# Kernel optimization log

Hardware: AMD Instinct MI355X
Metric: run time of the kernel (lower is better)

## Reference

```python
import jax, jax.numpy as jnp
import numpy as np

B, NQ, NK = 16, 1024, 1024
DQ = DK = DV = 512
H = 4
DH = DV // H  # 128


def layer_norm(x, g, b, eps=1e-5):
    mu = jnp.mean(x, axis=-1, keepdims=True)
    var = jnp.var(x, axis=-1, keepdims=True)  # biased, matches torch LayerNorm
    return (x - mu) / jnp.sqrt(var + eps) * g + b


def setup_inputs() -> dict:
    key = jax.random.key(0)
    ks = jax.random.split(key, 16)
    s = lambda d: 1.0 / np.sqrt(d)
    return {
        "Q": jax.random.normal(ks[0], (B, NQ, DQ), jnp.float32),
        "K": jax.random.normal(ks[1], (B, NK, DK), jnp.float32),
        "weights": jax.random.uniform(ks[2], (H * B, NQ, NK), jnp.float32),
        "Wq": jax.random.normal(ks[3], (DV, DQ), jnp.float32) * s(DQ),
        "bq": jnp.zeros((DV,), jnp.float32),
        "Wk": jax.random.normal(ks[4], (DV, DK), jnp.float32) * s(DK),
        "bk": jnp.zeros((DV,), jnp.float32),
        "Wv": jax.random.normal(ks[5], (DV, DK), jnp.float32) * s(DK),
        "bv": jnp.zeros((DV,), jnp.float32),
        "Wo": jax.random.normal(ks[6], (DV, DV), jnp.float32) * s(DV),
        "bo": jnp.zeros((DV,), jnp.float32),
        "g0": jnp.ones((DV,), jnp.float32),
        "beta0": jnp.zeros((DV,), jnp.float32),
        "g1": jnp.ones((DV,), jnp.float32),
        "beta1": jnp.zeros((DV,), jnp.float32),
    }


def reference(Q, K, weights, Wq, bq, Wk, bk, Wv, bv, Wo, bo, g0, beta0, g1, beta1):
    q = Q @ Wq.T + bq  # [B,NQ,DV]
    k = K @ Wk.T + bk  # [B,NK,DV]
    v = K @ Wv.T + bv  # [B,NK,DV]

    # torch split(dh, 2) + cat(0) == head-major [H,B,N,DH]
    def heads(x, n):
        return x.reshape(B, n, H, DH).transpose(2, 0, 1, 3)

    q_, k_, v_ = heads(q, NQ), heads(k, NK), heads(v, NK)

    # NOTE: original scales by sqrt(dim_V), not sqrt(head_dim)
    scores = jnp.einsum("hbqd,hbkd->hbqk", q_, k_) / np.sqrt(DV)
    log_w = jnp.log(jnp.clip(weights, 0.0, None)).reshape(H, B, NQ, NK)
    A = jax.nn.softmax(scores + log_w, axis=-1)  # [H,B,NQ,NK]

    o = q_ + jnp.einsum("hbqk,hbkd->hbqd", A, v_)  # residual inside heads
    # split(B,0)+cat(2) == merge heads back to [B,NQ,DV]
    O = o.transpose(1, 2, 0, 3).reshape(B, NQ, DV)
    O = layer_norm(O, g0, beta0)
    O = O + jax.nn.relu(O @ Wo.T + bo)
    O = layer_norm(O, g1, beta1)
    return O
```

## Files before the change

kernel.cpp:

```cpp
#include <hip/hip_runtime.h>

typedef unsigned short u16;
typedef unsigned int u32;
typedef __attribute__((ext_vector_type(8))) short short8;
typedef __attribute__((ext_vector_type(4))) float f32x4;
typedef __attribute__((ext_vector_type(2))) u32 uintx2;
typedef __attribute__((address_space(3))) u32 lds32;
typedef const __attribute__((address_space(1))) u32 g32c;

__device__ __forceinline__ u16 f2bf(float f) {
  union { float f; u32 u; } v; v.f = f;
  return (u16)((v.u + 0x7fffu + ((v.u >> 16) & 1u)) >> 16);
}
__device__ __forceinline__ float bf2f(u16 h) {
  union { u32 u; float f; } v; v.u = ((u32)h) << 16;
  return v.f;
}

__global__ void cvt_w_kernel(const float* __restrict__ Wq, const float* __restrict__ Wk,
                             const float* __restrict__ Wv, const float* __restrict__ Wo,
                             u16* __restrict__ dst) {
  int m = blockIdx.y;
  const float* s = (m == 0) ? Wq : (m == 1) ? Wk : (m == 2) ? Wv : Wo;
  int idx = (blockIdx.x * 256 + threadIdx.x) * 4;
  float4 v = *(const float4*)(s + idx);
  uintx2 pk;
  pk[0] = (u32)f2bf(v.x) | ((u32)f2bf(v.y) << 16);
  pk[1] = (u32)f2bf(v.z) | ((u32)f2bf(v.w) << 16);
  *(uintx2*)(dst + m * 262144 + idx) = pk;
}

template <bool AF32, bool OUTMODE, bool TRANSV>
__device__ __forceinline__ void gemm_bt_body(const void* __restrict__ Ap,
                                             const u16* __restrict__ Bw,
                                             const float* __restrict__ bias,
                                             u16* __restrict__ C) {
  __shared__ u16 ldsA[128 * 64];
  __shared__ u16 ldsB[128 * 64];
  const int t = threadIdx.x;
  const int lane = t & 63, wid = t >> 6;
  const int lr = lane & 15, lg = lane >> 4;
  const int n0 = blockIdx.x * 128;
  const int m0 = blockIdx.y * 128;
  const int wr = (wid >> 1) * 64, wc = (wid & 1) * 64;

  f32x4 acc[4][4];
#pragma unroll
  for (int i = 0; i < 4; ++i)
#pragma unroll
    for (int j = 0; j < 4; ++j)
#pragma unroll
      for (int r = 0; r < 4; ++r) acc[i][j][r] = 0.f;

  for (int kt = 0; kt < 512; kt += 64) {
    __syncthreads();
#pragma unroll
    for (int i = 0; i < 4; ++i) {
      int lin = i * 256 + t;
      int row = lin >> 3, u = lin & 7;
      int pu = u ^ (row & 7);
      if constexpr (AF32) {
        const float* src = (const float*)Ap + (size_t)(m0 + row) * 512 + kt + u * 8;
        float4 v0 = *(const float4*)src;
        float4 v1 = *(const float4*)(src + 4);
        short8 pk;
        pk[0] = (short)f2bf(v0.x); pk[1] = (short)f2bf(v0.y);
        pk[2] = (short)f2bf(v0.z); pk[3] = (short)f2bf(v0.w);
        pk[4] = (short)f2bf(v1.x); pk[5] = (short)f2bf(v1.y);
        pk[6] = (short)f2bf(v1.z); pk[7] = (short)f2bf(v1.w);
        *(short8*)&ldsA[row * 64 + pu * 8] = pk;
      } else {
        const u16* src = (const u16*)Ap + (size_t)(m0 + row) * 512 + kt + u * 8;
        *(short8*)&ldsA[row * 64 + pu * 8] = *(const short8*)src;
      }
      const u16* bsrc = Bw + (size_t)(n0 + row) * 512 + kt + u * 8;
      *(short8*)&ldsB[row * 64 + pu * 8] = *(const short8*)bsrc;
    }
    __syncthreads();
#pragma unroll
    for (int kk = 0; kk < 2; ++kk) {
      short8 af[4], bfr[4];
#pragma unroll
      for (int mf = 0; mf < 4; ++mf) {
        int row = wr + mf * 16 + lr;
        af[mf] = *(const short8*)&ldsA[row * 64 + (((kk * 4 + lg) ^ (row & 7)) * 8)];
      }
#pragma unroll
      for (int nf = 0; nf < 4; ++nf) {
        int row = wc + nf * 16 + lr;
        bfr[nf] = *(const short8*)&ldsB[row * 64 + (((kk * 4 + lg) ^ (row & 7)) * 8)];
      }
#pragma unroll
      for (int mf = 0; mf < 4; ++mf)
#pragma unroll
        for (int nf = 0; nf < 4; ++nf)
          acc[mf][nf] =
              __builtin_amdgcn_mfma_f32_16x16x32_bf16(af[mf], bfr[nf], acc[mf][nf], 0, 0, 0);
    }
  }

  if constexpr (TRANSV) {
    const int h_ = n0 >> 7;
#pragma unroll
    for (int mf = 0; mf < 4; ++mf)
#pragma unroll
      for (int nf = 0; nf < 4; ++nf) {
        int d = wc + nf * 16 + lr;
        int rr0 = m0 + wr + mf * 16 + lg * 4;
        int b_ = rr0 >> 10;
        int k0 = rr0 & 1023;
        float bvv = bias[n0 + d];
        uintx2 pk;
        pk[0] = (u32)f2bf(acc[mf][nf][0] + bvv) | ((u32)f2bf(acc[mf][nf][1] + bvv) << 16);
        pk[1] = (u32)f2bf(acc[mf][nf][2] + bvv) | ((u32)f2bf(acc[mf][nf][3] + bvv) << 16);
        *(uintx2*)(C + (((size_t)b_ * 4 + h_) * 128 + d) * 1024 + k0) = pk;
      }
  } else {
#pragma unroll
    for (int mf = 0; mf < 4; ++mf)
#pragma unroll
      for (int nf = 0; nf < 4; ++nf) {
        int c = n0 + wc + nf * 16 + lr;
        float bv = bias[c];
#pragma unroll
        for (int r = 0; r < 4; ++r) {
          int rr = m0 + wr + mf * 16 + lg * 4 + r;
          float v = acc[mf][nf][r] + bv;
          if constexpr (OUTMODE) {
            v = v > 0.f ? v : 0.f;
            v += bf2f(((const u16*)Ap)[(size_t)rr * 512 + c]);
          }
          C[(size_t)rr * 512 + c] = f2bf(v);
        }
      }
  }
}

__global__ __launch_bounds__(256) void gemm3_kernel(const float* __restrict__ Q,
                                                    const float* __restrict__ K,
                                                    const u16* __restrict__ Wb,
                                                    const float* __restrict__ bq,
                                                    const float* __restrict__ bk,
                                                    const float* __restrict__ bv,
                                                    u16* qb, u16* kb, u16* vbT) {
  int z = blockIdx.z;
  if (z == 2) {
    gemm_bt_body<true, false, true>(K, Wb + 524288, bv, vbT);
  } else {
    const void* Ap = (z == 0) ? (const void*)Q : (const void*)K;
    const u16* Bw = Wb + z * 262144;
    const float* bias = (z == 0) ? bq : bk;
    u16* C = (z == 0) ? qb : kb;
    gemm_bt_body<true, false, false>(Ap, Bw, bias, C);
  }
}

__global__ __launch_bounds__(256) void gemmo_kernel(const u16* __restrict__ X,
                                                    const u16* __restrict__ Wb,
                                                    const float* __restrict__ bo,
                                                    u16* Z) {
  gemm_bt_body<false, true, false>(X, Wb, bo, Z);
}

__global__ __launch_bounds__(256) void attn_kernel(const u16* __restrict__ qb,
                                                   const u16* __restrict__ kb,
                                                   const u16* __restrict__ vbT,
                                                   const float* __restrict__ Wt,
                                                   u16* __restrict__ Ob) {
  __shared__ __align__(16) u16 ldsK[2][64 * 128];
  __shared__ __align__(16) u16 ldsVT[2][128 * 64];
  __shared__ __align__(16) u16 ldsP[128 * 64];
  const int t = threadIdx.x;
  const int lane = t & 63, wid = t >> 6;
  const int lr = lane & 15, lg = lane >> 4;
  const int hb = blockIdx.y;
  const int b = hb & 15;
  const int h = hb >> 4;
  const int q0 = blockIdx.x * 128;
  const int wq = wid * 32;
  const size_t kvbase = ((size_t)b * 1024) * 512 + h * 128;
  const size_t vtbase = ((size_t)b * 4 + h) * 131072;
  const float SCALE = 0.044194173824159216f;

  const u16* ksrc[4];
  const u16* vtsrc[4];
#pragma unroll
  for (int i = 0; i < 4; ++i) {
    {
      int lin = i * 256 + t;
      int row = lin >> 4, u = lin & 15;
      ksrc[i] = kb + kvbase + (size_t)row * 512 + ((u ^ (row & 15)) * 8);
    }
    {
      int lin = i * 256 + t;
      int row = lin >> 3, u = lin & 7;
      vtsrc[i] = vbT + vtbase + (size_t)row * 1024 + ((u ^ (row & 7)) * 8);
    }
  }
  const int wslot = (t & 192) * 8;

#define STAGE(bu)                                                                           \
  do {                                                                                      \
    _Pragma("unroll") for (int i_ = 0; i_ < 4; ++i_) {                                      \
      __builtin_amdgcn_global_load_lds((g32c*)(ksrc[i_]),                                   \
                                       (lds32*)(&ldsK[bu][i_ * 2048 + wslot]), 16, 0, 0);   \
      __builtin_amdgcn_global_load_lds((g32c*)(vtsrc[i_]),                                  \
                                       (lds32*)(&ldsVT[bu][i_ * 2048 + wslot]), 16, 0, 0);  \
      ksrc[i_] += 32768;                                                \
      vtsrc[i_] += 64;                                                  \
    }                                                                                       \
  } while (0)

  const float* wp0 = Wt + ((size_t)hb * 1024 + q0 + wq + lr) * 1024 + lg * 4;
  const float* wp1 = wp0 + 16 * 1024;

#define WLOADP(W)                                          \
  do {                                                     \
    _Pragma("unroll") for (int j_ = 0; j_ < 4; ++j_) {     \
      W[j_]     = *(const f32x4*)(wp0 + j_ * 16);          \
      W[4 + j_] = *(const f32x4*)(wp1 + j_ * 16);          \
    }                                                      \
    wp0 += 64; wp1 += 64;                                  \
  } while (0)

  short8 qfr[2][4];
#pragma unroll
  for (int nf = 0; nf < 2; ++nf) {
    const u16* qp = qb + kvbase + (size_t)(q0 + wq + nf * 16 + lr) * 512 + lg * 8;
#pragma unroll
    for (int ds = 0; ds < 4; ++ds) qfr[nf][ds] = *(const short8*)(qp + ds * 32);
  }

  f32x4 oacc[2][8];
#pragma unroll
  for (int i = 0; i < 2; ++i)
#pragma unroll
    for (int j = 0; j < 8; ++j)
#pragma unroll
      for (int r = 0; r < 4; ++r) oacc[i][j][r] = 0.f;
  float lacc[2] = {0.f, 0.f};

  auto tile_compute = [&](const u16* bK, const u16* bVT, const f32x4 (&W)[8]) {
    f32x4 sacc[4][2];
#pragma unroll
    for (int i = 0; i < 4; ++i)
#pragma unroll
      for (int j = 0; j < 2; ++j)
#pragma unroll
        for (int r = 0; r < 4; ++r) sacc[i][j][r] = 0.f;

#pragma unroll
    for (int ds = 0; ds < 4; ++ds) {
      short8 kf[4];
#pragma unroll
      for (int mf = 0; mf < 4; ++mf) {
        int row = mf * 16 + lr;
        kf[mf] = *(const short8*)&bK[row * 128 + (((ds * 4 + lg) ^ (row & 15)) * 8)];
      }
#pragma unroll
      for (int mf = 0; mf < 4; ++mf)
#pragma unroll
        for (int nf = 0; nf < 2; ++nf)
          sacc[mf][nf] =
              __builtin_amdgcn_mfma_f32_16x16x32_bf16(kf[mf], qfr[nf][ds], sacc[mf][nf], 0, 0, 0);
    }

#pragma unroll
    for (int nf = 0; nf < 2; ++nf) {
      int prow = wq + nf * 16 + lr;
#pragma unroll
      for (int mf = 0; mf < 4; ++mf) {
        f32x4 w4 = W[nf * 4 + mf];
        float p0 = w4[0] * __expf(sacc[mf][nf][0] * SCALE);
        float p1 = w4[1] * __expf(sacc[mf][nf][1] * SCALE);
        float p2 = w4[2] * __expf(sacc[mf][nf][2] * SCALE);
        float p3 = w4[3] * __expf(sacc[mf][nf][3] * SCALE);
        lacc[nf] += (p0 + p1) + (p2 + p3);
        uintx2 pk;
        pk[0] = (u32)f2bf(p0) | ((u32)f2bf(p1) << 16);
        pk[1] = (u32)f2bf(p2) | ((u32)f2bf(p3) << 16);
        int byteoff = (prow * 128 + (mf * 16 + lg * 4) * 2) ^ ((prow & 7) << 4);
        *(uintx2*)((char*)ldsP + byteoff) = pk;
      }
    }

#pragma unroll
    for (int ks = 0; ks < 2; ++ks) {
      short8 pa[2];
#pragma unroll
      for (int qf = 0; qf < 2; ++qf) {
        int row = wq + qf * 16 + lr;
        int byteoff = (row * 128 + (ks * 4 + lg) * 16) ^ ((row & 7) << 4);
        pa[qf] = *(const short8*)((const char*)ldsP + byteoff);
      }
      short8 vf[8];
#pragma unroll
      for (int nf = 0; nf < 8; ++nf) {
        int row = nf * 16 + lr;
        vf[nf] = *(const short8*)&bVT[row * 64 + (((ks * 4 + lg) ^ (row & 7)) * 8)];
      }
#pragma unroll
      for (int qf = 0; qf < 2; ++qf)
#pragma unroll
        for (int nf = 0; nf < 8; ++nf)
          oacc[qf][nf] =
              __builtin_amdgcn_mfma_f32_16x16x32_bf16(pa[qf], vf[nf], oacc[qf][nf], 0, 0, 0);
    }
  };

#define SCHED_FENCE() __builtin_amdgcn_sched_barrier(0)
#define WAITBAR(N)                                                 \
  do {                                                             \
    SCHED_FENCE();                                                 \
    asm volatile("s_waitcnt vmcnt(" #N ")" ::: "memory");          \
    __builtin_amdgcn_s_barrier();                                  \
    SCHED_FENCE();                                                 \
  } while (0)
#define BAR()                                                      \
  do {                                                             \
    SCHED_FENCE();                                                 \
    __builtin_amdgcn_s_barrier();                                  \
    SCHED_FENCE();                                                 \
  } while (0)

  f32x4 wA[8], wB[8];
  WLOADP(wA);
  STAGE(0);

  for (int it = 0; it < 8; ++it) {
    {
      STAGE(1);
      WLOADP(wB);
      WAITBAR(16);
      tile_compute(&ldsK[0][0], &ldsVT[0][0], wA);
      BAR();
    }
    {
      if (it < 7) {
        STAGE(0);
        WLOADP(wA);
        WAITBAR(16);
      } else {
        WAITBAR(0);
      }
      tile_compute(&ldsK[1][0], &ldsVT[1][0], wB);
      if (it < 7) BAR();
    }
  }

  float lred[2];
#pragma unroll
  for (int nf = 0; nf < 2; ++nf) {
    float s = lacc[nf];
    s += __shfl_xor(s, 16);
    s += __shfl_xor(s, 32);
    lred[nf] = s;
  }

#pragma unroll
  for (int qf = 0; qf < 2; ++qf)
#pragma unroll
    for (int r = 0; r < 4; ++r) {
      float lv = __shfl(lred[qf], (lane & 48) | (lg * 4 + r));
      float linv = 1.0f / lv;
      int qrow = q0 + wq + qf * 16 + lg * 4 + r;
      size_t base = kvbase + (size_t)qrow * 512;
#pragma unroll
      for (int nf = 0; nf < 8; ++nf) {
        size_t idx = base + nf * 16 + lr;
        Ob[idx] = f2bf(bf2f(qb[idx]) + oacc[qf][nf][r] * linv);
      }
    }
#undef STAGE
#undef WLOADP
#undef WAITBAR
#undef BAR
#undef SCHED_FENCE
}

template <bool F32OUT>
__global__ __launch_bounds__(256) void ln_kernel(const u16* __restrict__ in,
                                                 const float* __restrict__ g,
                                                 const float* __restrict__ be,
                                                 void* __restrict__ outp) {
  const int lane = threadIdx.x & 63, wid = threadIdx.x >> 6;
  const int row = blockIdx.x * 4 + wid;
  const u16* p = in + (size_t)row * 512 + lane * 8;
  short8 v = *(const short8*)p;
  float x[8];
  float s = 0.f, s2 = 0.f;
#pragma unroll
  for (int j = 0; j < 8; ++j) {
    x[j] = bf2f((u16)v[j]);
    s += x[j];
    s2 += x[j] * x[j];
  }
#pragma unroll
  for (int off = 1; off < 64; off <<= 1) {
    s += __shfl_xor(s, off);
    s2 += __shfl_xor(s2, off);
  }
  float mu = s * (1.f / 512.f);
  float var = s2 * (1.f / 512.f) - mu * mu;
  float rs = rsqrtf(var + 1e-5f);
  float4 ga = *(const float4*)(g + lane * 8);
  float4 gb = *(const float4*)(g + lane * 8 + 4);
  float4 ba = *(const float4*)(be + lane * 8);
  float4 bb = *(const float4*)(be + lane * 8 + 4);
  float gg[8] = {ga.x, ga.y, ga.z, ga.w, gb.x, gb.y, gb.z, gb.w};
  float bv[8] = {ba.x, ba.y, ba.z, ba.w, bb.x, bb.y, bb.z, bb.w};
  if constexpr (F32OUT) {
    float* out = (float*)outp + (size_t)row * 512 + lane * 8;
    float4 o0, o1;
    o0.x = (x[0] - mu) * rs * gg[0] + bv[0];
    o0.y = (x[1] - mu) * rs * gg[1] + bv[1];
    o0.z = (x[2] - mu) * rs * gg[2] + bv[2];
    o0.w = (x[3] - mu) * rs * gg[3] + bv[3];
    o1.x = (x[4] - mu) * rs * gg[4] + bv[4];
    o1.y = (x[5] - mu) * rs * gg[5] + bv[5];
    o1.z = (x[6] - mu) * rs * gg[6] + bv[6];
    o1.w = (x[7] - mu) * rs * gg[7] + bv[7];
    *(float4*)out = o0;
    *(float4*)(out + 4) = o1;
  } else {
    short8 o;
#pragma unroll
    for (int j = 0; j < 8; ++j) o[j] = (short)f2bf((x[j] - mu) * rs * gg[j] + bv[j]);
    *(short8*)((u16*)outp + (size_t)row * 512 + lane * 8) = o;
  }
}

extern "C" void kernel_launch(void* const* d_in, const int* in_sizes, int n_in,
                              void* d_out, int out_size, void* d_ws, size_t ws_size,
                              hipStream_t stream) {
  (void)in_sizes; (void)n_in; (void)out_size; (void)ws_size;
  const float* Q   = (const float*)d_in[0];
  const float* K   = (const float*)d_in[1];
  const float* Wt  = (const float*)d_in[2];
  const float* Wq  = (const float*)d_in[3];
  const float* bq  = (const float*)d_in[4];
  const float* Wk  = (const float*)d_in[5];
  const float* bk  = (const float*)d_in[6];
  const float* Wv  = (const float*)d_in[7];
  const float* bv  = (const float*)d_in[8];
  const float* Wo  = (const float*)d_in[9];
  const float* bo  = (const float*)d_in[10];
  const float* g0  = (const float*)d_in[11];
  const float* be0 = (const float*)d_in[12];
  const float* g1  = (const float*)d_in[13];
  const float* be1 = (const float*)d_in[14];

  char* ws = (char*)d_ws;
  const size_t MB16 = 16777216;
  u16* qb  = (u16*)(ws);
  u16* kb  = (u16*)(ws + MB16);
  u16* vbT = (u16*)(ws + 2 * MB16);
  u16* Wb  = (u16*)(ws + 3 * MB16);
  u16* Ob  = (u16*)d_out;

  cvt_w_kernel<<<dim3(256, 4), 256, 0, stream>>>(Wq, Wk, Wv, Wo, Wb);
  gemm3_kernel<<<dim3(4, 128, 3), 256, 0, stream>>>(Q, K, Wb, bq, bk, bv, qb, kb, vbT);
  attn_kernel<<<dim3(8, 64), 256, 0, stream>>>(qb, kb, vbT, Wt, Ob);
  ln_kernel<false><<<4096, 256, 0, stream>>>(Ob, g0, be0, qb);
  gemmo_kernel<<<dim3(4, 128), 256, 0, stream>>>(qb, Wb + 786432, bo, kb);
  ln_kernel<true><<<4096, 256, 0, stream>>>(kb, g1, be1, d_out);
}
```

Before: 249.8 us.

## Shrink attention tiles to 64 queries and 32 keys for higher occupancy

The attention kernel now gives each block 64 query rows (16 per wave) and walks keys in 32-row tiles, so it launches twice as many blocks. The P buffer is padded instead of XOR-swizzled, the launch bound asks for 3 blocks per CU, and MFMA sections are wrapped in s_setprio. The aim is to fill the GPU better and hide latency through more resident waves. In exchange, each block does less reuse of the K/V tiles it loads, so global and LDS traffic per FLOP rises, and there are twice as many barriers per key pass.

```diff
diff --git a/kernel.cpp b/kernel.cpp
--- a/kernel.cpp
+++ b/kernel.cpp
@@ -162,30 +162,30 @@
   gemm_bt_body<false, true, false>(X, Wb, bo, Z);
 }
 
-__global__ __launch_bounds__(256) void attn_kernel(const u16* __restrict__ qb,
-                                                   const u16* __restrict__ kb,
-                                                   const u16* __restrict__ vbT,
-                                                   const float* __restrict__ Wt,
-                                                   u16* __restrict__ Ob) {
-  __shared__ __align__(16) u16 ldsK[2][64 * 128];
-  __shared__ __align__(16) u16 ldsVT[2][128 * 64];
-  __shared__ __align__(16) u16 ldsP[128 * 64];
+__global__ __launch_bounds__(256, 3) void attn_kernel(const u16* __restrict__ qb,
+                                                      const u16* __restrict__ kb,
+                                                      const u16* __restrict__ vbT,
+                                                      const float* __restrict__ Wt,
+                                                      u16* __restrict__ Ob) {
+  __shared__ __align__(16) u16 ldsK[2][32 * 128];
+  __shared__ __align__(16) u16 ldsVT[2][128 * 32];
+  __shared__ __align__(16) u16 ldsP[64 * 40];
   const int t = threadIdx.x;
   const int lane = t & 63, wid = t >> 6;
   const int lr = lane & 15, lg = lane >> 4;
   const int hb = blockIdx.y;
   const int b = hb & 15;
   const int h = hb >> 4;
-  const int q0 = blockIdx.x * 128;
-  const int wq = wid * 32;
+  const int q0 = blockIdx.x * 64;
+  const int wq = wid * 16;
   const size_t kvbase = ((size_t)b * 1024) * 512 + h * 128;
   const size_t vtbase = ((size_t)b * 4 + h) * 131072;
   const float SCALE = 0.044194173824159216f;
 
-  const u16* ksrc[4];
-  const u16* vtsrc[4];
-#pragma unroll
-  for (int i = 0; i < 4; ++i) {
+  const u16* ksrc[2];
+  const u16* vtsrc[2];
+#pragma unroll
+  for (int i = 0; i < 2; ++i) {
     {
       int lin = i * 256 + t;
       int row = lin >> 4, u = lin & 15;
@@ -193,119 +193,96 @@
     }
     {
       int lin = i * 256 + t;
-      int row = lin >> 3, u = lin & 7;
-      vtsrc[i] = vbT + vtbase + (size_t)row * 1024 + ((u ^ (row & 7)) * 8);
+      int row = lin >> 2, u = lin & 3;
+      vtsrc[i] = vbT + vtbase + (size_t)row * 1024 + ((u ^ (row & 3)) * 8);
     }
   }
   const int wslot = (t & 192) * 8;
 
 #define STAGE(bu)                                                                           \
   do {                                                                                      \
-    _Pragma("unroll") for (int i_ = 0; i_ < 4; ++i_) {                                      \
+    _Pragma("unroll") for (int i_ = 0; i_ < 2; ++i_) {                                      \
       __builtin_amdgcn_global_load_lds((g32c*)(ksrc[i_]),                                   \
                                        (lds32*)(&ldsK[bu][i_ * 2048 + wslot]), 16, 0, 0);   \
       __builtin_amdgcn_global_load_lds((g32c*)(vtsrc[i_]),                                  \
                                        (lds32*)(&ldsVT[bu][i_ * 2048 + wslot]), 16, 0, 0);  \
-      ksrc[i_] += 32768;                                                \
-      vtsrc[i_] += 64;                                                  \
+      ksrc[i_] += 16384;                                                \
+      vtsrc[i_] += 32;                                                  \
     }                                                                                       \
   } while (0)
 
-  const float* wp0 = Wt + ((size_t)hb * 1024 + q0 + wq + lr) * 1024 + lg * 4;
-  const float* wp1 = wp0 + 16 * 1024;
-
-#define WLOADP(W)                                          \
-  do {                                                     \
-    _Pragma("unroll") for (int j_ = 0; j_ < 4; ++j_) {     \
-      W[j_]     = *(const f32x4*)(wp0 + j_ * 16);          \
-      W[4 + j_] = *(const f32x4*)(wp1 + j_ * 16);          \
-    }                                                      \
-    wp0 += 64; wp1 += 64;                                  \
+  const float* wp = Wt + ((size_t)hb * 1024 + q0 + wq + lr) * 1024 + lg * 4;
+
+#define WLOADP(W)                        \
+  do {                                   \
+    W[0] = *(const f32x4*)(wp);          \
+    W[1] = *(const f32x4*)(wp + 16);     \
+    wp += 32;                            \
   } while (0)
 
-  short8 qfr[2][4];
-#pragma unroll
-  for (int nf = 0; nf < 2; ++nf) {
-    const u16* qp = qb + kvbase + (size_t)(q0 + wq + nf * 16 + lr) * 512 + lg * 8;
-#pragma unroll
-    for (int ds = 0; ds < 4; ++ds) qfr[nf][ds] = *(const short8*)(qp + ds * 32);
-  }
-
-  f32x4 oacc[2][8];
-#pragma unroll
-  for (int i = 0; i < 2; ++i)
-#pragma unroll
-    for (int j = 0; j < 8; ++j)
-#pragma unroll
-      for (int r = 0; r < 4; ++r) oacc[i][j][r] = 0.f;
-  float lacc[2] = {0.f, 0.f};
-
-  auto tile_compute = [&](const u16* bK, const u16* bVT, const f32x4 (&W)[8]) {
-    f32x4 sacc[4][2];
-#pragma unroll
-    for (int i = 0; i < 4; ++i)
-#pragma unroll
-      for (int j = 0; j < 2; ++j)
-#pragma unroll
-        for (int r = 0; r < 4; ++r) sacc[i][j][r] = 0.f;
+  short8 qfr[4];
+  {
+    const u16* qp = qb + kvbase + (size_t)(q0 + wq + lr) * 512 + lg * 8;
+#pragma unroll
+    for (int ds = 0; ds < 4; ++ds) qfr[ds] = *(const short8*)(qp + ds * 32);
+  }
+
+  f32x4 oacc[8];
+#pragma unroll
+  for (int j = 0; j < 8; ++j)
+#pragma unroll
+    for (int r = 0; r < 4; ++r) oacc[j][r] = 0.f;
+  float lacc = 0.f;
+
+  auto tile_compute = [&](const u16* bK, const u16* bVT, const f32x4 (&W)[2]) {
+    f32x4 sacc[2];
+#pragma unroll
+    for (int j = 0; j < 2; ++j)
+#pragma unroll
+      for (int r = 0; r < 4; ++r) sacc[j][r] = 0.f;
 
 #pragma unroll
     for (int ds = 0; ds < 4; ++ds) {
-      short8 kf[4];
-#pragma unroll
-      for (int mf = 0; mf < 4; ++mf) {
+      short8 kf[2];
+#pragma unroll
+      for (int mf = 0; mf < 2; ++mf) {
         int row = mf * 16 + lr;
         kf[mf] = *(const short8*)&bK[row * 128 + (((ds * 4 + lg) ^ (row & 15)) * 8)];
       }
-#pragma unroll
-      for (int mf = 0; mf < 4; ++mf)
-#pragma unroll
-        for (int nf = 0; nf < 2; ++nf)
-          sacc[mf][nf] =
-              __builtin_amdgcn_mfma_f32_16x16x32_bf16(kf[mf], qfr[nf][ds], sacc[mf][nf], 0, 0, 0);
-    }
-
-#pragma unroll
-    for (int nf = 0; nf < 2; ++nf) {
-      int prow = wq + nf * 16 + lr;
-#pragma unroll
-      for (int mf = 0; mf < 4; ++mf) {
-        f32x4 w4 = W[nf * 4 + mf];
-        float p0 = w4[0] * __expf(sacc[mf][nf][0] * SCALE);
-        float p1 = w4[1] * __expf(sacc[mf][nf][1] * SCALE);
-        float p2 = w4[2] * __expf(sacc[mf][nf][2] * SCALE);
-        float p3 = w4[3] * __expf(sacc[mf][nf][3] * SCALE);
-        lacc[nf] += (p0 + p1) + (p2 + p3);
-        uintx2 pk;
-        pk[0] = (u32)f2bf(p0) | ((u32)f2bf(p1) << 16);
-        pk[1] = (u32)f2bf(p2) | ((u32)f2bf(p3) << 16);
-        int byteoff = (prow * 128 + (mf * 16 + lg * 4) * 2) ^ ((prow & 7) << 4);
-        *(uintx2*)((char*)ldsP + byteoff) = pk;
-      }
-    }
-
-#pragma unroll
-    for (int ks = 0; ks < 2; ++ks) {
-      short8 pa[2];
-#pragma unroll
-      for (int qf = 0; qf < 2; ++qf) {
-        int row = wq + qf * 16 + lr;
-        int byteoff = (row * 128 + (ks * 4 + lg) * 16) ^ ((row & 7) << 4);
-        pa[qf] = *(const short8*)((const char*)ldsP + byteoff);
-      }
-      short8 vf[8];
-#pragma unroll
-      for (int nf = 0; nf < 8; ++nf) {
-        int row = nf * 16 + lr;
-        vf[nf] = *(const short8*)&bVT[row * 64 + (((ks * 4 + lg) ^ (row & 7)) * 8)];
-      }
-#pragma unroll
-      for (int qf = 0; qf < 2; ++qf)
-#pragma unroll
-        for (int nf = 0; nf < 8; ++nf)
-          oacc[qf][nf] =
-              __builtin_amdgcn_mfma_f32_16x16x32_bf16(pa[qf], vf[nf], oacc[qf][nf], 0, 0, 0);
-    }
+      __builtin_amdgcn_s_setprio(1);
+#pragma unroll
+      for (int mf = 0; mf < 2; ++mf)
+        sacc[mf] = __builtin_amdgcn_mfma_f32_16x16x32_bf16(kf[mf], qfr[ds], sacc[mf], 0, 0, 0);
+      __builtin_amdgcn_s_setprio(0);
+    }
+
+    const int prow = wq + lr;
+#pragma unroll
+    for (int mf = 0; mf < 2; ++mf) {
+      f32x4 w4 = W[mf];
+      float p0 = w4[0] * __expf(sacc[mf][0] * SCALE);
+      float p1 = w4[1] * __expf(sacc[mf][1] * SCALE);
+      float p2 = w4[2] * __expf(sacc[mf][2] * SCALE);
+      float p3 = w4[3] * __expf(sacc[mf][3] * SCALE);
+      lacc += (p0 + p1) + (p2 + p3);
+      uintx2 pk;
+      pk[0] = (u32)f2bf(p0) | ((u32)f2bf(p1) << 16);
+      pk[1] = (u32)f2bf(p2) | ((u32)f2bf(p3) << 16);
+      *(uintx2*)((char*)ldsP + prow * 80 + mf * 32 + lg * 8) = pk;
+    }
+
+    short8 pa = *(const short8*)((const char*)ldsP + (wq + lr) * 80 + lg * 16);
+    short8 vf[8];
+#pragma unroll
+    for (int nf = 0; nf < 8; ++nf) {
+      int row = nf * 16 + lr;
+      vf[nf] = *(const short8*)&bVT[row * 32 + ((lg ^ (row & 3)) * 8)];
+    }
+    __builtin_amdgcn_s_setprio(1);
+#pragma unroll
+    for (int nf = 0; nf < 8; ++nf)
+      oacc[nf] = __builtin_amdgcn_mfma_f32_16x16x32_bf16(pa, vf[nf], oacc[nf], 0, 0, 0);
+    __builtin_amdgcn_s_setprio(0);
   };
 
 #define SCHED_FENCE() __builtin_amdgcn_sched_barrier(0)
@@ -323,54 +300,47 @@
     SCHED_FENCE();                                                 \
   } while (0)
 
-  f32x4 wA[8], wB[8];
+  f32x4 wA[2], wB[2];
   WLOADP(wA);
   STAGE(0);
 
-  for (int it = 0; it < 8; ++it) {
+  for (int it = 0; it < 16; ++it) {
     {
       STAGE(1);
       WLOADP(wB);
-      WAITBAR(16);
+      WAITBAR(6);
       tile_compute(&ldsK[0][0], &ldsVT[0][0], wA);
       BAR();
     }
     {
-      if (it < 7) {
+      if (it < 15) {
         STAGE(0);
         WLOADP(wA);
-        WAITBAR(16);
+        WAITBAR(6);
       } else {
         WAITBAR(0);
       }
       tile_compute(&ldsK[1][0], &ldsVT[1][0], wB);
-      if (it < 7) BAR();
-    }
-  }
-
-  float lred[2];
-#pragma unroll
-  for (int nf = 0; nf < 2; ++nf) {
-    float s = lacc[nf];
-    s += __shfl_xor(s, 16);
-    s += __shfl_xor(s, 32);
-    lred[nf] = s;
-  }
-
-#pragma unroll
-  for (int qf = 0; qf < 2; ++qf)
-#pragma unroll
-    for (int r = 0; r < 4; ++r) {
-      float lv = __shfl(lred[qf], (lane & 48) | (lg * 4 + r));
-      float linv = 1.0f / lv;
-      int qrow = q0 + wq + qf * 16 + lg * 4 + r;
-      size_t base = kvbase + (size_t)qrow * 512;
-#pragma unroll
-      for (int nf = 0; nf < 8; ++nf) {
-        size_t idx = base + nf * 16 + lr;
-        Ob[idx] = f2bf(bf2f(qb[idx]) + oacc[qf][nf][r] * linv);
-      }
-    }
+      if (it < 15) BAR();
+    }
+  }
+
+  float lred = lacc;
+  lred += __shfl_xor(lred, 16);
+  lred += __shfl_xor(lred, 32);
+
+#pragma unroll
+  for (int r = 0; r < 4; ++r) {
+    float lv = __shfl(lred, (lane & 48) | (lg * 4 + r));
+    float linv = 1.0f / lv;
+    int qrow = q0 + wq + lg * 4 + r;
+    size_t base = kvbase + (size_t)qrow * 512;
+#pragma unroll
+    for (int nf = 0; nf < 8; ++nf) {
+      size_t idx = base + nf * 16 + lr;
+      Ob[idx] = f2bf(bf2f(qb[idx]) + oacc[nf][r] * linv);
+    }
+  }
 #undef STAGE
 #undef WLOADP
 #undef WAITBAR
@@ -460,7 +430,7 @@
 
   cvt_w_kernel<<<dim3(256, 4), 256, 0, stream>>>(Wq, Wk, Wv, Wo, Wb);
   gemm3_kernel<<<dim3(4, 128, 3), 256, 0, stream>>>(Q, K, Wb, bq, bk, bv, qb, kb, vbT);
-  attn_kernel<<<dim3(8, 64), 256, 0, stream>>>(qb, kb, vbT, Wt, Ob);
+  attn_kernel<<<dim3(16, 64), 256, 0, stream>>>(qb, kb, vbT, Wt, Ob);
   ln_kernel<false><<<4096, 256, 0, stream>>>(Ob, g0, be0, qb);
   gemmo_kernel<<<dim3(4, 128), 256, 0, stream>>>(qb, Wb + 786432, bo, kb);
   ln_kernel<true><<<4096, 256, 0, stream>>>(kb, g1, be1, d_out);
```

After: 258.1 us. 1.03x slower.
